# Kernel tuning notes

Measured on AMD Instinct MI355X. Metric: run time of the kernel, lower is better.

## Reference

```python
import jax, jax.numpy as jnp
import numpy as np

B, N, D, H = 8, 1024, 512, 8
DK = D // H  # key_dim == val_dim == 64
LN_EPS = 1e-5


def setup_inputs() -> dict:
    key = jax.random.key(0)
    ks = jax.random.split(key, 16)
    stdv = 1.0 / np.sqrt(D)
    u = lambda k, shape, s: jax.random.uniform(k, shape, jnp.float32, -s, s)
    inp = {
        'q': jax.random.normal(ks[0], (B, N, D), jnp.float32),
        'mask': jax.random.uniform(ks[1], (B, N, N)) < 0.1,  # True = masked out
        # eps1 is torch.zeros in the source (never re-initialized); use small
        'eps1': jax.random.normal(ks[2], (D, D), jnp.float32) * 0.03,
        # 3 MLP layers, stacked on leading axis. Linear: y = x @ W.T + b
        'U_w': u(ks[3], (3, D, D), stdv), 'U_b': u(ks[4], (3, D), stdv),
        'V_w': u(ks[5], (3, D, D), stdv), 'V_b': u(ks[6], (3, D), stdv),
        'ln_g': jnp.ones((3, D), jnp.float32), 'ln_b': jnp.zeros((3, D), jnp.float32),
        'W_query': u(ks[7], (H, D, DK), 1.0 / np.sqrt(DK)),
        'W_key':   u(ks[8], (H, D, DK), 1.0 / np.sqrt(DK)),
        'W_val':   u(ks[9], (H, D, DK), 1.0 / np.sqrt(DK)),
        'W_out':   u(ks[10], (H, DK, D), stdv),
    }
    return inp


def _layer_norm(x, g, b):
    mu = jnp.mean(x, axis=-1, keepdims=True)
    var = jnp.mean(jnp.square(x - mu), axis=-1, keepdims=True)
    return (x - mu) * jax.lax.rsqrt(var + LN_EPS) * g + b


def _mlp_layer(x, Uw, Ub, Vw, Vb, g, b):
    # U1 -> (identity maxpool k=1) -> V1 -> LayerNorm -> ReLU -> residual
    y = x @ Uw.T + Ub
    y = y @ Vw.T + Vb
    y = _layer_norm(y, g, b)
    return x + jax.nn.relu(y)


def reference(q, mask, eps1, U_w, U_b, V_w, V_b, ln_g, ln_b,
              W_query, W_key, W_val, W_out):
    nf = 1.0 / np.sqrt(DK)  # norm_factor; applied to BOTH Q and K as in source
    h = q
    for l in range(3):
        h = _mlp_layer(h @ eps1, U_w[l], U_b[l], V_w[l], V_b[l], ln_g[l], ln_b[l])
    # per-head projections: (H,B,N,DK)
    Q = jnp.einsum('bqd,hdk->hbqk', q, W_query) * nf
    K = jnp.einsum('bgd,hdk->hbgk', h, W_key) * nf
    V = jnp.einsum('bgd,hdk->hbgk', h, W_val)
    scores = jnp.einsum('hbqk,hbgk->hbqg', Q, K)  # (H,B,N,N)
    scores = jnp.where(mask[None], -1e10, scores)
    attn = jax.nn.softmax(scores, axis=-1)
    heads = jnp.einsum('hbqg,hbgv->hbqv', attn, V)
    out = jnp.einsum('hbqv,hvd->bqd', heads, W_out)  # (B,N,D)
    return out
```

## Files before the change

kernel.cpp:

```cpp
#include <hip/hip_runtime.h>

typedef __attribute__((ext_vector_type(8))) short bhalf8;
typedef __attribute__((ext_vector_type(4))) float f32x4;

__device__ __forceinline__ ushort f2bf(float f) {
  unsigned u = __builtin_bit_cast(unsigned, f);
  unsigned r = u + 0x7fffu + ((u >> 16) & 1u);
  return (ushort)(r >> 16);
}

__device__ __forceinline__ void gld16(const ushort* g, ushort* l) {
  __builtin_amdgcn_global_load_lds((const __attribute__((address_space(1))) void*)g,
                                   (__attribute__((address_space(3))) void*)l, 16, 0, 0);
}

__global__ __launch_bounds__(256) void prep_kernel(
    const float* __restrict__ q, const int* __restrict__ mask,
    const float* __restrict__ eps1, const float* __restrict__ U_w,
    const float* __restrict__ V_w, const float* __restrict__ Wq,
    const float* __restrict__ Wk, const float* __restrict__ Wv,
    const float* __restrict__ Wo,
    ushort* __restrict__ qb, unsigned long long* __restrict__ mbits,
    ushort* __restrict__ uwb, ushort* __restrict__ vwb,
    ushort* __restrict__ e1b, ushort* __restrict__ e1t,
    ushort* __restrict__ wqkv, ushort* __restrict__ wot) {
  int i = blockIdx.x * 256 + threadIdx.x;
  if (i < 4194304) {
    qb[i] = f2bf(q[i]);
  } else if (i < 12582912) {
    int j = i - 4194304;
    unsigned long long bb = __ballot(mask[j] != 0);
    if ((threadIdx.x & 63) == 0) {
      int b = j >> 20, qq = (j >> 10) & 1023, g = j & 1023;
      mbits[((size_t)b * 16 + (g >> 6)) * 1024 + qq] = bb;
    }
  } else if (i < 13369344) {
    int j = i - 12582912;
    uwb[j] = f2bf(U_w[j]);
  } else if (i < 14155776) {
    int j = i - 13369344;
    vwb[j] = f2bf(V_w[j]);
  } else if (i < 14417920) {
    int j = i - 14155776;
    e1b[j] = f2bf(eps1[j]);
  } else if (i < 14680064) {
    int j = i - 14417920; int n = j >> 9, k = j & 511;
    e1t[j] = f2bf(eps1[k * 512 + n]);
  } else if (i < 15466496) {
    int j = i - 14680064; int n = j >> 9, d = j & 511;
    const float* W = (n < 512) ? Wq : (n < 1024 ? Wk : Wv);
    float sc = (n < 512) ? 0.02255252509f : 1.0f;
    int nl = n & 511;
    wqkv[j] = f2bf(W[((nl >> 6) * 512 + d) * 64 + (nl & 63)] * sc);
  } else if (i < 15728640) {
    int j = i - 15466496; int d = j >> 9, hv = j & 511;
    wot[j] = f2bf(Wo[hv * 512 + d]);
  }
}

__global__ __launch_bounds__(256) void cvec_kernel(
    const float* __restrict__ U_b, const float* __restrict__ V_w,
    const float* __restrict__ V_b, float* __restrict__ cvec) {
  int idx = blockIdx.x * 4 + (threadIdx.x >> 6);
  int lane = threadIdx.x & 63;
  int l = idx >> 9;
  const float* vr = V_w + (size_t)idx * 512 + lane * 8;
  const float* ur = U_b + l * 512 + lane * 8;
  float s = 0;
#pragma unroll
  for (int i = 0; i < 8; i++) s += vr[i] * ur[i];
#pragma unroll
  for (int off = 1; off < 64; off <<= 1) s += __shfl_xor(s, off, 64);
  if (lane == 0) cvec[idx] = s + V_b[idx];
}

template <int BN>
__global__ __launch_bounds__(256) void gemm_nt(
    const ushort* __restrict__ A0, const ushort* __restrict__ A1,
    const ushort* __restrict__ Bt0, const ushort* __restrict__ Bt1,
    int bsplit, int mstride, int M, int K,
    ushort* __restrict__ O0, const float* __restrict__ b0,
    ushort* __restrict__ O1, const float* __restrict__ b1,
    ushort* __restrict__ O2, const float* __restrict__ b2,
    float* __restrict__ F0, float* __restrict__ F1, int vtreg) {
  __shared__ ushort As[128 * 32];
  __shared__ ushort Bs[BN * 32];
  int tid = threadIdx.x;
  int wave = tid >> 6, lane = tid & 63;
  int quad = lane >> 4, col = lane & 15;
  int m0 = blockIdx.y * 128, n0 = blockIdx.x * BN;
  const ushort* A = (A1 && n0 >= 512) ? A1 : A0;
  const ushort* Bp = ((n0 < bsplit) ? Bt0 + (size_t)n0 * K
                                    : Bt1 + (size_t)(n0 - bsplit) * K) +
                     (size_t)(m0 >> 9) * mstride;
  constexpr int NI = BN / 32;
  int wm = (BN == 128) ? (wave >> 1) * 64 : (wave & 1) * 64;
  int wn = (BN == 128) ? (wave & 1) * 64 : (wave >> 1) * 32;
  f32x4 acc[4][NI] = {};
  int srow = wave * 16 + (lane >> 2);
  int skc = (lane & 3) * 8;
  const ushort* gA0 = A + (size_t)(m0 + srow) * K + skc;
  const ushort* gA1 = gA0 + (size_t)64 * K;
  const ushort* gB0 = Bp + (size_t)srow * K + skc;
  const ushort* gB1 = gB0 + (size_t)64 * K;
  ushort* lA0 = &As[wave * 16 * 32];
  ushort* lA1 = &As[(64 + wave * 16) * 32];
  ushort* lB0 = &Bs[wave * 16 * 32];
  ushort* lB1 = (BN == 128) ? &Bs[(64 + wave * 16) * 32] : nullptr;

  gld16(gA0, lA0);
  gld16(gA1, lA1);
  gld16(gB0, lB0);
  if (BN == 128) gld16(gB1, lB1);

  for (int k0 = 0; k0 < K; k0 += 32) {
    __syncthreads();
    bhalf8 af[4], bg[NI];
#pragma unroll
    for (int i = 0; i < 4; i++)
      af[i] = *(bhalf8*)&As[(wm + i * 16 + col) * 32 + quad * 8];
#pragma unroll
    for (int i = 0; i < NI; i++)
      bg[i] = *(bhalf8*)&Bs[(wn + i * 16 + col) * 32 + quad * 8];
    __syncthreads();
    if (k0 + 32 < K) {
      gld16(gA0 + k0 + 32, lA0);
      gld16(gA1 + k0 + 32, lA1);
      gld16(gB0 + k0 + 32, lB0);
      if (BN == 128) gld16(gB1 + k0 + 32, lB1);
    }
#pragma unroll
    for (int mi = 0; mi < 4; mi++)
#pragma unroll
      for (int ni = 0; ni < NI; ni++)
        acc[mi][ni] = __builtin_amdgcn_mfma_f32_16x16x32_bf16(af[mi], bg[ni], acc[mi][ni], 0, 0, 0);
  }

  int reg = n0 >> 9;
  ushort* Oreg = (reg == 0) ? O0 : (reg == 1 ? O1 : O2);
  const float* breg = (reg == 0) ? b0 : (reg == 1 ? b1 : b2);
  float* Freg = (reg == 0) ? F0 : (reg == 1 ? F1 : nullptr);
  bool vt = (reg == vtreg);
#pragma unroll
  for (int mi = 0; mi < 4; mi++)
#pragma unroll
    for (int ni = 0; ni < NI; ni++) {
      int cn = n0 + wn + ni * 16 + col;
      int cnl = cn & 511;
      int cmb = m0 + wm + mi * 16 + quad * 4;
      float bv = breg ? breg[cnl] : 0.f;
      if (vt) {
        ushort4 pk;
        pk.x = f2bf(acc[mi][ni][0] + bv);
        pk.y = f2bf(acc[mi][ni][1] + bv);
        pk.z = f2bf(acc[mi][ni][2] + bv);
        pk.w = f2bf(acc[mi][ni][3] + bv);
        *(ushort4*)&O2[((size_t)((cmb >> 10) * 512 + cnl)) * 1024 + (cmb & 1023)] = pk;
      } else if (Freg) {
#pragma unroll
        for (int r = 0; r < 4; r++)
          Freg[(size_t)(cmb + r) * 512 + cnl] = acc[mi][ni][r] + bv;
      } else {
#pragma unroll
        for (int r = 0; r < 4; r++)
          Oreg[(size_t)(cmb + r) * 512 + cnl] = f2bf(acc[mi][ni][r] + bv);
      }
    }
}

__global__ __launch_bounds__(256) void ln_kernel(
    const float* __restrict__ z, const float* __restrict__ t,
    const float* __restrict__ lgam, const float* __restrict__ lbet,
    ushort* __restrict__ hb) {
  int row = blockIdx.x * 4 + (threadIdx.x >> 6);
  int lane = threadIdx.x & 63;
  int cbase = lane * 8;
  const float* zr = z + (size_t)row * 512 + cbase;
  float x[8];
  *(float4*)&x[0] = *(const float4*)zr;
  *(float4*)&x[4] = *(const float4*)(zr + 4);
  float sum = 0;
#pragma unroll
  for (int i = 0; i < 8; i++) sum += x[i];
#pragma unroll
  for (int off = 1; off < 64; off <<= 1) sum += __shfl_xor(sum, off, 64);
  float mu = sum * (1.f / 512.f);
  float vs = 0;
#pragma unroll
  for (int i = 0; i < 8; i++) { float d = x[i] - mu; vs += d * d; }
#pragma unroll
  for (int off = 1; off < 64; off <<= 1) vs += __shfl_xor(vs, off, 64);
  float rstd = rsqrtf(vs * (1.f / 512.f) + 1e-5f);
  const float* tr = t + (size_t)row * 512 + cbase;
  float tv[8];
  *(float4*)&tv[0] = *(const float4*)tr;
  *(float4*)&tv[4] = *(const float4*)(tr + 4);
  ushort outv[8];
#pragma unroll
  for (int i = 0; i < 8; i++) {
    float val = (x[i] - mu) * rstd * lgam[cbase + i] + lbet[cbase + i];
    outv[i] = f2bf(tv[i] + fmaxf(val, 0.f));
  }
  *(uint4*)&hb[(size_t)row * 512 + cbase] = *(uint4*)outv;
}

__global__ __launch_bounds__(256) void attn_kernel(
    const ushort* __restrict__ Qp, const ushort* __restrict__ Kp,
    const ushort* __restrict__ VtG, const unsigned long long* __restrict__ mbits,
    ushort* __restrict__ Op) {
  int bh = blockIdx.x, qt = blockIdx.y;
  int b = bh >> 3, h = bh & 7;
  __shared__ ushort Ks[64 * 72];
  __shared__ ushort Vts[64 * 72];
  __shared__ ushort Ps[4][16 * 72];
  int tid = threadIdx.x, wave = tid >> 6, lane = tid & 63;
  int quad = lane >> 4, col = lane & 15;
  int q0 = qt * 64;
  bhalf8 aq[2];
  {
    const ushort* qr = &Qp[(size_t)(b * 1024 + q0 + wave * 16 + col) * 512 + h * 64 + quad * 8];
    aq[0] = *(const bhalf8*)qr;
    aq[1] = *(const bhalf8*)(qr + 32);
  }
  f32x4 o[4] = {};
  float lsum[4] = {0.f, 0.f, 0.f, 0.f};
  int srow = tid >> 3, svc = (tid & 7) * 8;
  int qrow0 = q0 + wave * 16 + quad * 4;
  const ushort* kbase = &Kp[(size_t)(b * 1024 + srow) * 512 + h * 64 + svc];
  const ushort* vbase = &VtG[(size_t)(bh * 64 + srow) * 1024 + svc];
  uint4 pk0 = *(const uint4*)(kbase);
  uint4 pk1 = *(const uint4*)(kbase + (size_t)32 * 512);
  uint4 pv0 = *(const uint4*)(vbase);
  uint4 pv1 = *(const uint4*)(vbase + (size_t)32 * 1024);

  for (int g0 = 0; g0 < 1024; g0 += 64) {
    __syncthreads();
    *(uint4*)&Ks[srow * 72 + svc] = pk0;
    *(uint4*)&Ks[(srow + 32) * 72 + svc] = pk1;
    *(uint4*)&Vts[srow * 72 + svc] = pv0;
    *(uint4*)&Vts[(srow + 32) * 72 + svc] = pv1;
    __syncthreads();
    if (g0 + 64 < 1024) {
      pk0 = *(const uint4*)(kbase + (size_t)(g0 + 64) * 512);
      pk1 = *(const uint4*)(kbase + (size_t)(g0 + 96) * 512);
      pv0 = *(const uint4*)(vbase + g0 + 64);
      pv1 = *(const uint4*)(vbase + (size_t)32 * 1024 + g0 + 64);
    }
    f32x4 s[4] = {};
#pragma unroll
    for (int nt = 0; nt < 4; nt++)
#pragma unroll
      for (int kk = 0; kk < 2; kk++) {
        bhalf8 bk = *(bhalf8*)&Ks[(nt * 16 + col) * 72 + kk * 32 + quad * 8];
        s[nt] = __builtin_amdgcn_mfma_f32_16x16x32_bf16(aq[kk], bk, s[nt], 0, 0, 0);
      }
    const unsigned long long* mp = &mbits[((size_t)b * 16 + (g0 >> 6)) * 1024 + qrow0];
    unsigned long long mw0 = mp[0], mw1 = mp[1], mw2 = mp[2], mw3 = mp[3];
#pragma unroll
    for (int r = 0; r < 4; r++) {
      unsigned long long mw = (r == 0) ? mw0 : (r == 1 ? mw1 : (r == 2 ? mw2 : mw3));
      unsigned lo = (unsigned)mw, hi = (unsigned)(mw >> 32);
#pragma unroll
      for (int nt = 0; nt < 4; nt++) {
        unsigned word = (nt < 2) ? lo : hi;
        unsigned sh = (nt & 1) ? (col + 16) : col;
        unsigned keep = ((word >> sh) & 1u) - 1u;
        float p = exp2f(s[nt][r]);
        float pm = __builtin_bit_cast(float, __builtin_bit_cast(unsigned, p) & keep);
        lsum[r] += pm;
        Ps[wave][(quad * 4 + r) * 72 + nt * 16 + col] = f2bf(pm);
      }
    }
    bhalf8 ap[2];
#pragma unroll
    for (int kk = 0; kk < 2; kk++)
      ap[kk] = *(bhalf8*)&Ps[wave][col * 72 + kk * 32 + quad * 8];
#pragma unroll
    for (int vt = 0; vt < 4; vt++)
#pragma unroll
      for (int kk = 0; kk < 2; kk++) {
        bhalf8 bv = *(bhalf8*)&Vts[(vt * 16 + col) * 72 + kk * 32 + quad * 8];
        o[vt] = __builtin_amdgcn_mfma_f32_16x16x32_bf16(ap[kk], bv, o[vt], 0, 0, 0);
      }
  }
  float rl[4];
#pragma unroll
  for (int r = 0; r < 4; r++) {
#pragma unroll
    for (int off = 1; off < 16; off <<= 1) lsum[r] += __shfl_xor(lsum[r], off, 64);
    rl[r] = __builtin_amdgcn_rcpf(lsum[r]);
  }
#pragma unroll
  for (int vt = 0; vt < 4; vt++)
#pragma unroll
    for (int r = 0; r < 4; r++) {
      int qrow = qrow0 + r;
      int v = vt * 16 + col;
      Op[(size_t)(b * 1024 + qrow) * 512 + h * 64 + v] = f2bf(o[vt][r] * rl[r]);
    }
}

extern "C" void kernel_launch(void* const* d_in, const int* in_sizes, int n_in,
                              void* d_out, int out_size, void* d_ws, size_t ws_size,
                              hipStream_t stream) {
  const float* q    = (const float*)d_in[0];
  const int*   mask = (const int*)d_in[1];
  const float* eps1 = (const float*)d_in[2];
  const float* U_w  = (const float*)d_in[3];
  const float* U_b  = (const float*)d_in[4];
  const float* V_w  = (const float*)d_in[5];
  const float* V_b  = (const float*)d_in[6];
  const float* ln_g = (const float*)d_in[7];
  const float* ln_b = (const float*)d_in[8];
  const float* Wq   = (const float*)d_in[9];
  const float* Wk   = (const float*)d_in[10];
  const float* Wv   = (const float*)d_in[11];
  const float* Wo   = (const float*)d_in[12];
  float* out = (float*)d_out;

  char* ws = (char*)d_ws;
  auto carve = [&](size_t bytes) { char* p = ws; ws += bytes; return p; };
  ushort* qb   = (ushort*)carve(8388608);
  ushort* uwb  = (ushort*)carve(1572864);
  ushort* vwb  = (ushort*)carve(1572864);
  ushort* e1b  = (ushort*)carve(524288);
  ushort* e1t  = (ushort*)carve(524288);
  ushort* wqkv = (ushort*)carve(1572864);
  ushort* wot  = (ushort*)carve(524288);
  ushort* A1b  = (ushort*)carve(1572864);
  ushort* Gtb  = (ushort*)carve(1572864);
  float*  cvec = (float*)carve(6144);
  unsigned long long* mbits = (unsigned long long*)carve(1048576);
  float*  tf   = (float*)carve(16777216);
  float*  zf   = (float*)carve(16777216);
  ushort* hb   = (ushort*)carve(8388608);
  ushort* Qb   = (ushort*)carve(8388608);
  ushort* Kb   = (ushort*)carve(8388608);
  ushort* VtG  = (ushort*)carve(8388608);
  ushort* Ob   = (ushort*)carve(8388608);
  const int BIG = 1 << 30;

  prep_kernel<<<61440, 256, 0, stream>>>(q, mask, eps1, U_w, V_w, Wq, Wk, Wv, Wo,
                                         qb, mbits, uwb, vwb, e1b, e1t, wqkv, wot);
  cvec_kernel<<<384, 256, 0, stream>>>(U_b, V_w, V_b, cvec);
  gemm_nt<128><<<dim3(12, 4), 256, 0, stream>>>(
      e1b, nullptr, uwb, nullptr, BIG, 0, 512, 512,
      A1b, nullptr, A1b + 262144, nullptr, A1b + 524288, nullptr,
      nullptr, nullptr, -1);
  gemm_nt<64><<<dim3(8, 12), 256, 0, stream>>>(
      vwb, nullptr, A1b, nullptr, BIG, 262144, 1536, 512,
      Gtb, nullptr, nullptr, nullptr, nullptr, nullptr,
      nullptr, nullptr, -1);
  const ushort* hsrc = qb;
  for (int l = 0; l < 3; l++) {
    gemm_nt<128><<<dim3(8, 64), 256, 0, stream>>>(
        hsrc, nullptr, e1t, Gtb + l * 262144, 512, 0, 8192, 512,
        nullptr, nullptr, nullptr, cvec + l * 512, nullptr, nullptr,
        tf, zf, -1);
    ln_kernel<<<2048, 256, 0, stream>>>(zf, tf, ln_g + l * 512, ln_b + l * 512, hb);
    hsrc = hb;
  }
  gemm_nt<128><<<dim3(12, 64), 256, 0, stream>>>(
      qb, hb, wqkv, nullptr, BIG, 0, 8192, 512,
      Qb, nullptr, Kb, nullptr, VtG, nullptr, nullptr, nullptr, 2);
  attn_kernel<<<dim3(64, 16), 256, 0, stream>>>(Qb, Kb, VtG, mbits, Ob);
  gemm_nt<64><<<dim3(8, 64), 256, 0, stream>>>(
      Ob, nullptr, wot, nullptr, BIG, 0, 8192, 512,
      nullptr, nullptr, nullptr, nullptr, nullptr, nullptr, out, nullptr, -1);
}
```

Before: 322.0 us.

## Restructure attention to split keys across waves and merge cvec into prep

The attention kernel now has each wave own a slice of the keys for all 64 queries. K and V fragments load straight from global memory into registers, and partial outputs are reduced across waves through shared memory at the end. The row sum comes from an extra MFMA against a ones vector, and a new repack kernel transposes the mask bits to match this access pattern. Other changes fold the cvec computation into the prep kernel, store the GEMM's t output as bf16 instead of fp32 to cut memory traffic in the LN step, and swap the GEMM grid axes so consecutive blocks walk along M. The risks are the cost of the cross-wave reduction, the extra repack launch, and bf16 rounding on the residual path.

```diff
diff --git a/kernel.cpp b/kernel.cpp
--- a/kernel.cpp
+++ b/kernel.cpp
@@ -19,11 +19,13 @@
     const float* __restrict__ eps1, const float* __restrict__ U_w,
     const float* __restrict__ V_w, const float* __restrict__ Wq,
     const float* __restrict__ Wk, const float* __restrict__ Wv,
-    const float* __restrict__ Wo,
+    const float* __restrict__ Wo, const float* __restrict__ U_b,
+    const float* __restrict__ V_b,
     ushort* __restrict__ qb, unsigned long long* __restrict__ mbits,
     ushort* __restrict__ uwb, ushort* __restrict__ vwb,
     ushort* __restrict__ e1b, ushort* __restrict__ e1t,
-    ushort* __restrict__ wqkv, ushort* __restrict__ wot) {
+    ushort* __restrict__ wqkv, ushort* __restrict__ wot,
+    float* __restrict__ cvec) {
   int i = blockIdx.x * 256 + threadIdx.x;
   if (i < 4194304) {
     qb[i] = f2bf(q[i]);
@@ -55,23 +57,34 @@
   } else if (i < 15728640) {
     int j = i - 15466496; int d = j >> 9, hv = j & 511;
     wot[j] = f2bf(Wo[hv * 512 + d]);
-  }
-}
-
-__global__ __launch_bounds__(256) void cvec_kernel(
-    const float* __restrict__ U_b, const float* __restrict__ V_w,
-    const float* __restrict__ V_b, float* __restrict__ cvec) {
-  int idx = blockIdx.x * 4 + (threadIdx.x >> 6);
+  } else {
+    int j = i - 15728640;
+    int idx = j >> 6, ln = j & 63;
+    int l = idx >> 9;
+    const float* vr = V_w + (size_t)idx * 512 + ln * 8;
+    const float* ur = U_b + l * 512 + ln * 8;
+    float s = 0;
+#pragma unroll
+    for (int t = 0; t < 8; t++) s += vr[t] * ur[t];
+#pragma unroll
+    for (int off = 1; off < 64; off <<= 1) s += __shfl_xor(s, off, 64);
+    if (ln == 0) cvec[idx] = s + V_b[idx];
+  }
+}
+
+__global__ __launch_bounds__(256) void mrepack_kernel(
+    const unsigned long long* __restrict__ mbits,
+    unsigned long long* __restrict__ mT) {
+  int id = blockIdx.x * 4 + (threadIdx.x >> 6);
   int lane = threadIdx.x & 63;
-  int l = idx >> 9;
-  const float* vr = V_w + (size_t)idx * 512 + lane * 8;
-  const float* ur = U_b + l * 512 + lane * 8;
-  float s = 0;
-#pragma unroll
-  for (int i = 0; i < 8; i++) s += vr[i] * ur[i];
-#pragma unroll
-  for (int off = 1; off < 64; off <<= 1) s += __shfl_xor(s, off, 64);
-  if (lane == 0) cvec[idx] = s + V_b[idx];
+  int b = id >> 8, gw = (id >> 4) & 15, qw = id & 15;
+  unsigned long long row = mbits[((size_t)b * 16 + gw) * 1024 + qw * 64 + lane];
+  unsigned long long keep = 0;
+  for (int j = 0; j < 64; j++) {
+    unsigned long long bal = __ballot((row >> j) & 1ull);
+    if (lane == j) keep = bal;
+  }
+  mT[((size_t)b * 1024 + gw * 64 + lane) * 16 + qw] = keep;
 }
 
 template <int BN>
@@ -88,7 +101,7 @@
   int tid = threadIdx.x;
   int wave = tid >> 6, lane = tid & 63;
   int quad = lane >> 4, col = lane & 15;
-  int m0 = blockIdx.y * 128, n0 = blockIdx.x * BN;
+  int m0 = blockIdx.x * 128, n0 = blockIdx.y * BN;
   const ushort* A = (A1 && n0 >= 512) ? A1 : A0;
   const ushort* Bp = ((n0 < bsplit) ? Bt0 + (size_t)n0 * K
                                     : Bt1 + (size_t)(n0 - bsplit) * K) +
@@ -169,7 +182,7 @@
 }
 
 __global__ __launch_bounds__(256) void ln_kernel(
-    const float* __restrict__ z, const float* __restrict__ t,
+    const float* __restrict__ z, const ushort* __restrict__ tb,
     const float* __restrict__ lgam, const float* __restrict__ lbet,
     ushort* __restrict__ hb) {
   int row = blockIdx.x * 4 + (threadIdx.x >> 6);
@@ -191,10 +204,16 @@
 #pragma unroll
   for (int off = 1; off < 64; off <<= 1) vs += __shfl_xor(vs, off, 64);
   float rstd = rsqrtf(vs * (1.f / 512.f) + 1e-5f);
-  const float* tr = t + (size_t)row * 512 + cbase;
+  uint4 tr = *(const uint4*)&tb[(size_t)row * 512 + cbase];
   float tv[8];
-  *(float4*)&tv[0] = *(const float4*)tr;
-  *(float4*)&tv[4] = *(const float4*)(tr + 4);
+  {
+    const unsigned* u = (const unsigned*)&tr;
+#pragma unroll
+    for (int w = 0; w < 4; w++) {
+      tv[2 * w] = __builtin_bit_cast(float, u[w] << 16);
+      tv[2 * w + 1] = __builtin_bit_cast(float, u[w] & 0xFFFF0000u);
+    }
+  }
   ushort outv[8];
 #pragma unroll
   for (int i = 0; i < 8; i++) {
@@ -204,100 +223,122 @@
   *(uint4*)&hb[(size_t)row * 512 + cbase] = *(uint4*)outv;
 }
 
-__global__ __launch_bounds__(256) void attn_kernel(
+__global__ __launch_bounds__(256, 2) void attn_kernel(
     const ushort* __restrict__ Qp, const ushort* __restrict__ Kp,
-    const ushort* __restrict__ VtG, const unsigned long long* __restrict__ mbits,
+    const ushort* __restrict__ VtG, const unsigned long long* __restrict__ mT,
     ushort* __restrict__ Op) {
   int bh = blockIdx.x, qt = blockIdx.y;
   int b = bh >> 3, h = bh & 7;
-  __shared__ ushort Ks[64 * 72];
-  __shared__ ushort Vts[64 * 72];
-  __shared__ ushort Ps[4][16 * 72];
+  __shared__ __align__(16) char pool[21504];
   int tid = threadIdx.x, wave = tid >> 6, lane = tid & 63;
   int quad = lane >> 4, col = lane & 15;
   int q0 = qt * 64;
-  bhalf8 aq[2];
+  ushort* Ps = (ushort*)pool + wave * 2560;
+
+  bhalf8 aq[4][2];
   {
-    const ushort* qr = &Qp[(size_t)(b * 1024 + q0 + wave * 16 + col) * 512 + h * 64 + quad * 8];
-    aq[0] = *(const bhalf8*)qr;
-    aq[1] = *(const bhalf8*)(qr + 32);
-  }
-  f32x4 o[4] = {};
-  float lsum[4] = {0.f, 0.f, 0.f, 0.f};
-  int srow = tid >> 3, svc = (tid & 7) * 8;
-  int qrow0 = q0 + wave * 16 + quad * 4;
-  const ushort* kbase = &Kp[(size_t)(b * 1024 + srow) * 512 + h * 64 + svc];
-  const ushort* vbase = &VtG[(size_t)(bh * 64 + srow) * 1024 + svc];
-  uint4 pk0 = *(const uint4*)(kbase);
-  uint4 pk1 = *(const uint4*)(kbase + (size_t)32 * 512);
-  uint4 pv0 = *(const uint4*)(vbase);
-  uint4 pv1 = *(const uint4*)(vbase + (size_t)32 * 1024);
-
-  for (int g0 = 0; g0 < 1024; g0 += 64) {
+    const ushort* qbase = &Qp[(size_t)(b * 1024 + q0 + col) * 512 + h * 64 + quad * 8];
+#pragma unroll
+    for (int qs = 0; qs < 4; qs++) {
+      aq[qs][0] = *(const bhalf8*)(qbase + (size_t)(qs * 16) * 512);
+      aq[qs][1] = *(const bhalf8*)(qbase + (size_t)(qs * 16) * 512 + 32);
+    }
+  }
+  bhalf8 ones;
+  {
+    short v = (col == 0) ? (short)0x3F80 : (short)0;
+#pragma unroll
+    for (int j = 0; j < 8; j++) ones[j] = v;
+  }
+  f32x4 o[4][5] = {};
+  const ushort* kbase = &Kp[(size_t)(b * 1024 + col) * 512 + h * 64 + quad * 8];
+  const ushort* vbase = &VtG[(size_t)(bh * 64 + col) * 1024];
+  int gsel = (quad >> 1) * 64 + (quad & 1) * 8;
+
+  for (int g0 = 0; g0 < 1024; g0 += 128) {
+    int gA = g0 + wave * 16;
+    bhalf8 bk[2][2];
+    bk[0][0] = *(const bhalf8*)(kbase + (size_t)gA * 512);
+    bk[0][1] = *(const bhalf8*)(kbase + (size_t)gA * 512 + 32);
+    bk[1][0] = *(const bhalf8*)(kbase + (size_t)(gA + 64) * 512);
+    bk[1][1] = *(const bhalf8*)(kbase + (size_t)(gA + 64) * 512 + 32);
+    bhalf8 bv[4];
+#pragma unroll
+    for (int vs = 0; vs < 4; vs++)
+      bv[vs] = *(const bhalf8*)(vbase + (size_t)(vs * 16) * 1024 + g0 + wave * 16 + gsel);
+    unsigned long long inv0 = ~(mT[(size_t)(b * 1024 + gA + col) * 16 + qt] >> (quad * 4));
+    unsigned long long inv1 = ~(mT[(size_t)(b * 1024 + gA + 64 + col) * 16 + qt] >> (quad * 4));
+    unsigned i0lo = (unsigned)inv0, i0hi = (unsigned)(inv0 >> 32);
+    unsigned i1lo = (unsigned)inv1, i1hi = (unsigned)(inv1 >> 32);
+#pragma unroll
+    for (int qs = 0; qs < 4; qs++) {
+      f32x4 s0 = {}, s1 = {};
+      s0 = __builtin_amdgcn_mfma_f32_16x16x32_bf16(aq[qs][0], bk[0][0], s0, 0, 0, 0);
+      s0 = __builtin_amdgcn_mfma_f32_16x16x32_bf16(aq[qs][1], bk[0][1], s0, 0, 0, 0);
+      s1 = __builtin_amdgcn_mfma_f32_16x16x32_bf16(aq[qs][0], bk[1][0], s1, 0, 0, 0);
+      s1 = __builtin_amdgcn_mfma_f32_16x16x32_bf16(aq[qs][1], bk[1][1], s1, 0, 0, 0);
+      unsigned w0 = (qs < 2) ? i0lo : i0hi;
+      unsigned w1 = (qs < 2) ? i1lo : i1hi;
+#pragma unroll
+      for (int r = 0; r < 4; r++) {
+        int pos = (qs & 1) * 16 + r;
+        unsigned k0 = (unsigned)((int)(w0 << (31 - pos)) >> 31);
+        unsigned k1 = (unsigned)((int)(w1 << (31 - pos)) >> 31);
+        unsigned p0 = __builtin_bit_cast(unsigned, __builtin_amdgcn_exp2f(s0[r])) & k0;
+        unsigned p1 = __builtin_bit_cast(unsigned, __builtin_amdgcn_exp2f(s1[r])) & k1;
+        Ps[(qs * 16 + quad * 4 + r) * 40 + col] = (ushort)((p0 + 0x8000u) >> 16);
+        Ps[(qs * 16 + quad * 4 + r) * 40 + 16 + col] = (ushort)((p1 + 0x8000u) >> 16);
+      }
+    }
+#pragma unroll
+    for (int qs = 0; qs < 4; qs++) {
+      bhalf8 ap = *(const bhalf8*)&Ps[(qs * 16 + col) * 40 + quad * 8];
+#pragma unroll
+      for (int vs = 0; vs < 4; vs++)
+        o[qs][vs] = __builtin_amdgcn_mfma_f32_16x16x32_bf16(ap, bv[vs], o[qs][vs], 0, 0, 0);
+      o[qs][4] = __builtin_amdgcn_mfma_f32_16x16x32_bf16(ap, ones, o[qs][4], 0, 0, 0);
+    }
+  }
+  float* R = (float*)pool;
+  for (int src = 1; src < 4; src++) {
     __syncthreads();
-    *(uint4*)&Ks[srow * 72 + svc] = pk0;
-    *(uint4*)&Ks[(srow + 32) * 72 + svc] = pk1;
-    *(uint4*)&Vts[srow * 72 + svc] = pv0;
-    *(uint4*)&Vts[(srow + 32) * 72 + svc] = pv1;
+    if (wave == src) {
+      float* dst = R + lane * 84;
+#pragma unroll
+      for (int qs = 0; qs < 4; qs++)
+#pragma unroll
+        for (int vs = 0; vs < 5; vs++)
+          *(f32x4*)(dst + (qs * 5 + vs) * 4) = o[qs][vs];
+    }
     __syncthreads();
-    if (g0 + 64 < 1024) {
-      pk0 = *(const uint4*)(kbase + (size_t)(g0 + 64) * 512);
-      pk1 = *(const uint4*)(kbase + (size_t)(g0 + 96) * 512);
-      pv0 = *(const uint4*)(vbase + g0 + 64);
-      pv1 = *(const uint4*)(vbase + (size_t)32 * 1024 + g0 + 64);
-    }
-    f32x4 s[4] = {};
-#pragma unroll
-    for (int nt = 0; nt < 4; nt++)
-#pragma unroll
-      for (int kk = 0; kk < 2; kk++) {
-        bhalf8 bk = *(bhalf8*)&Ks[(nt * 16 + col) * 72 + kk * 32 + quad * 8];
-        s[nt] = __builtin_amdgcn_mfma_f32_16x16x32_bf16(aq[kk], bk, s[nt], 0, 0, 0);
+    if (wave == 0) {
+      const float* sp = R + lane * 84;
+#pragma unroll
+      for (int qs = 0; qs < 4; qs++)
+#pragma unroll
+        for (int vs = 0; vs < 5; vs++)
+          o[qs][vs] += *(const f32x4*)(sp + (qs * 5 + vs) * 4);
+    }
+  }
+  if (wave == 0) {
+#pragma unroll
+    for (int qs = 0; qs < 4; qs++) {
+      float rl[4];
+#pragma unroll
+      for (int r = 0; r < 4; r++) {
+        float lv = __shfl(o[qs][4][r], lane & 48, 64);
+        rl[r] = __builtin_amdgcn_rcpf(lv);
       }
-    const unsigned long long* mp = &mbits[((size_t)b * 16 + (g0 >> 6)) * 1024 + qrow0];
-    unsigned long long mw0 = mp[0], mw1 = mp[1], mw2 = mp[2], mw3 = mp[3];
-#pragma unroll
-    for (int r = 0; r < 4; r++) {
-      unsigned long long mw = (r == 0) ? mw0 : (r == 1 ? mw1 : (r == 2 ? mw2 : mw3));
-      unsigned lo = (unsigned)mw, hi = (unsigned)(mw >> 32);
-#pragma unroll
-      for (int nt = 0; nt < 4; nt++) {
-        unsigned word = (nt < 2) ? lo : hi;
-        unsigned sh = (nt & 1) ? (col + 16) : col;
-        unsigned keep = ((word >> sh) & 1u) - 1u;
-        float p = exp2f(s[nt][r]);
-        float pm = __builtin_bit_cast(float, __builtin_bit_cast(unsigned, p) & keep);
-        lsum[r] += pm;
-        Ps[wave][(quad * 4 + r) * 72 + nt * 16 + col] = f2bf(pm);
-      }
-    }
-    bhalf8 ap[2];
-#pragma unroll
-    for (int kk = 0; kk < 2; kk++)
-      ap[kk] = *(bhalf8*)&Ps[wave][col * 72 + kk * 32 + quad * 8];
-#pragma unroll
-    for (int vt = 0; vt < 4; vt++)
-#pragma unroll
-      for (int kk = 0; kk < 2; kk++) {
-        bhalf8 bv = *(bhalf8*)&Vts[(vt * 16 + col) * 72 + kk * 32 + quad * 8];
-        o[vt] = __builtin_amdgcn_mfma_f32_16x16x32_bf16(ap[kk], bv, o[vt], 0, 0, 0);
-      }
-  }
-  float rl[4];
-#pragma unroll
-  for (int r = 0; r < 4; r++) {
-#pragma unroll
-    for (int off = 1; off < 16; off <<= 1) lsum[r] += __shfl_xor(lsum[r], off, 64);
-    rl[r] = __builtin_amdgcn_rcpf(lsum[r]);
-  }
-#pragma unroll
-  for (int vt = 0; vt < 4; vt++)
-#pragma unroll
-    for (int r = 0; r < 4; r++) {
-      int qrow = qrow0 + r;
-      int v = vt * 16 + col;
-      Op[(size_t)(b * 1024 + qrow) * 512 + h * 64 + v] = f2bf(o[vt][r] * rl[r]);
-    }
+#pragma unroll
+      for (int vs = 0; vs < 4; vs++)
+#pragma unroll
+        for (int r = 0; r < 4; r++) {
+          int qrow = q0 + qs * 16 + quad * 4 + r;
+          Op[(size_t)(b * 1024 + qrow) * 512 + h * 64 + vs * 16 + col] =
+              f2bf(o[qs][vs][r] * rl[r]);
+        }
+    }
+  }
 }
 
 extern "C" void kernel_launch(void* const* d_in, const int* in_sizes, int n_in,
@@ -331,7 +372,8 @@
   ushort* Gtb  = (ushort*)carve(1572864);
   float*  cvec = (float*)carve(6144);
   unsigned long long* mbits = (unsigned long long*)carve(1048576);
-  float*  tf   = (float*)carve(16777216);
+  unsigned long long* mT    = (unsigned long long*)carve(2097152);
+  ushort* tb   = (ushort*)carve(8388608);
   float*  zf   = (float*)carve(16777216);
   ushort* hb   = (ushort*)carve(8388608);
   ushort* Qb   = (ushort*)carve(8388608);
@@ -340,31 +382,32 @@
   ushort* Ob   = (ushort*)carve(8388608);
   const int BIG = 1 << 30;
 
-  prep_kernel<<<61440, 256, 0, stream>>>(q, mask, eps1, U_w, V_w, Wq, Wk, Wv, Wo,
-                                         qb, mbits, uwb, vwb, e1b, e1t, wqkv, wot);
-  cvec_kernel<<<384, 256, 0, stream>>>(U_b, V_w, V_b, cvec);
-  gemm_nt<128><<<dim3(12, 4), 256, 0, stream>>>(
+  prep_kernel<<<61824, 256, 0, stream>>>(q, mask, eps1, U_w, V_w, Wq, Wk, Wv, Wo,
+                                         U_b, V_b, qb, mbits, uwb, vwb, e1b, e1t,
+                                         wqkv, wot, cvec);
+  mrepack_kernel<<<512, 256, 0, stream>>>(mbits, mT);
+  gemm_nt<128><<<dim3(4, 12), 256, 0, stream>>>(
       e1b, nullptr, uwb, nullptr, BIG, 0, 512, 512,
       A1b, nullptr, A1b + 262144, nullptr, A1b + 524288, nullptr,
       nullptr, nullptr, -1);
-  gemm_nt<64><<<dim3(8, 12), 256, 0, stream>>>(
+  gemm_nt<64><<<dim3(12, 8), 256, 0, stream>>>(
       vwb, nullptr, A1b, nullptr, BIG, 262144, 1536, 512,
       Gtb, nullptr, nullptr, nullptr, nullptr, nullptr,
       nullptr, nullptr, -1);
   const ushort* hsrc = qb;
   for (int l = 0; l < 3; l++) {
-    gemm_nt<128><<<dim3(8, 64), 256, 0, stream>>>(
+    gemm_nt<128><<<dim3(64, 8), 256, 0, stream>>>(
         hsrc, nullptr, e1t, Gtb + l * 262144, 512, 0, 8192, 512,
-        nullptr, nullptr, nullptr, cvec + l * 512, nullptr, nullptr,
-        tf, zf, -1);
-    ln_kernel<<<2048, 256, 0, stream>>>(zf, tf, ln_g + l * 512, ln_b + l * 512, hb);
+        tb, nullptr, nullptr, cvec + l * 512, nullptr, nullptr,
+        nullptr, zf, -1);
+    ln_kernel<<<2048, 256, 0, stream>>>(zf, tb, ln_g + l * 512, ln_b + l * 512, hb);
     hsrc = hb;
   }
-  gemm_nt<128><<<dim3(12, 64), 256, 0, stream>>>(
+  gemm_nt<128><<<dim3(64, 12), 256, 0, stream>>>(
       qb, hb, wqkv, nullptr, BIG, 0, 8192, 512,
       Qb, nullptr, Kb, nullptr, VtG, nullptr, nullptr, nullptr, 2);
-  attn_kernel<<<dim3(64, 16), 256, 0, stream>>>(Qb, Kb, VtG, mbits, Ob);
-  gemm_nt<64><<<dim3(8, 64), 256, 0, stream>>>(
+  attn_kernel<<<dim3(64, 16), 256, 0, stream>>>(Qb, Kb, VtG, mT, Ob);
+  gemm_nt<64><<<dim3(64, 8), 256, 0, stream>>>(
       Ob, nullptr, wot, nullptr, BIG, 0, 8192, 512,
       nullptr, nullptr, nullptr, nullptr, nullptr, nullptr, out, nullptr, -1);
 }
```

Result: no change. 318.5 us (-1.1%).
